# Optimization experiments

Hardware: AMD Instinct MI355X
Metric: run time of the kernel (lower is better)

## Reference

```python
import jax, jax.numpy as jnp
import numpy as np

ALPHA = 0.2          # LeakyReLU slope
NEG_BIG = -9e15      # mask value from the torch code
LN_EPS = 1e-5        # torch LayerNorm default eps
GAT_SCALE = 1.0


def _layer_norm(x, g, b):
    mu = x.mean(-1, keepdims=True)
    var = ((x - mu) ** 2).mean(-1, keepdims=True)
    return (x - mu) * jax.lax.rsqrt(var + LN_EPS) * g + b


def _gat_layer(h, adj, W, a, concat):
    # h: [B,N,Fin], adj: [N,N] weighted, W: [Fin,Fout], a: [2*Fout,1]
    Wh = jnp.einsum('bnf,fo->bno', h, W)                 # [B,N,Fout]
    Fo = W.shape[1]
    a_i, a_j = a[:Fo, 0], a[Fo:, 0]
    # e[b,i,j] = leakyrelu(Wh[b,i].a_i + Wh[b,j].a_j)  (== cat([Wh_i,Wh_j]) @ a)
    e = jax.nn.leaky_relu(
        (Wh @ a_i)[:, :, None] + (Wh @ a_j)[:, None, :], ALPHA)  # [B,N,N]
    att = jnp.where(adj[None, :, :] > 0, e, NEG_BIG)
    att = jax.nn.softmax(att, axis=2)
    att = att * adj[None, :, :]
    att = att / (att.sum(axis=2, keepdims=True) + 1e-8)
    h_prime = jnp.einsum('bij,bjo->bio', att, Wh)        # [B,N,Fout]
    return jax.nn.elu(h_prime) if concat else h_prime


def setup_inputs() -> dict:
    B, N, H, ID = 1024, 128, 64, 8
    GIN = 1 + ID  # node_feat_dim = 0
    key = jax.random.key(0)
    ks = jax.random.split(key, 20)
    # sparse weighted adjacency with self-loops
    w = jax.random.uniform(ks[0], (N, N))
    m = (jax.random.uniform(ks[1], (N, N)) < 0.3).astype(jnp.float32)
    adj = w * m + jnp.eye(N, dtype=jnp.float32)
    sc = lambda k, s: jax.random.normal(k, s, jnp.float32) * 0.1
    return {
        'c_values': jax.random.normal(ks[2], (B, N), jnp.float32),
        'adj': adj,
        'agent_emb': sc(ks[3], (N, ID)),
        'W1': sc(ks[4], (GIN, H)), 'a1': sc(ks[5], (2 * H, 1)),
        'W2': sc(ks[6], (H, H)),   'a2': sc(ks[7], (2 * H, 1)),
        'ln1_g': jnp.ones((H,)), 'ln1_b': jnp.zeros((H,)),
        'ln2_g': jnp.ones((H,)), 'ln2_b': jnp.zeros((H,)),
        'head_gat_w': sc(ks[8], (H, 1)), 'head_gat_b': jnp.zeros((1,)),
        'mlp1_w': sc(ks[9], (N, H)),  'mlp1_b': jnp.zeros((H,)),
        'mlp2_w': sc(ks[10], (H, H)), 'mlp2_b': jnp.zeros((H,)),
        'head_mlp_w': sc(ks[11], (H, 1)), 'head_mlp_b': jnp.zeros((1,)),
        'gate1_w': sc(ks[12], (N, H)), 'gate1_b': jnp.zeros((H,)),
        'gate2_w': sc(ks[13], (H, 1)), 'gate2_b': jnp.full((1,), -5.0),
    }


def reference(c_values, adj, agent_emb, W1, a1, W2, a2,
              ln1_g, ln1_b, ln2_g, ln2_b, head_gat_w, head_gat_b,
              mlp1_w, mlp1_b, mlp2_w, mlp2_b, head_mlp_w, head_mlp_b,
              gate1_w, gate1_b, gate2_w, gate2_b):
    B, N = c_values.shape
    # node features: [c_value, agent_id_embedding]
    id_feat = jnp.broadcast_to(agent_emb[None], (B, N, agent_emb.shape[1]))
    x_g = jnp.concatenate([c_values[..., None], id_feat], axis=-1)  # [B,N,9]
    h1 = _gat_layer(x_g, adj, W1, a1, concat=True)
    h1 = _layer_norm(h1, ln1_g, ln1_b)
    h2 = _gat_layer(h1, adj, W2, a2, concat=False)
    h = jax.nn.relu(h2 + h1)
    h = _layer_norm(h, ln2_g, ln2_b)
    q_gat = h.mean(axis=1) @ head_gat_w + head_gat_b                # [B,1]
    x_m = jax.nn.relu(c_values @ mlp1_w + mlp1_b)
    x_m = jax.nn.relu(x_m @ mlp2_w + mlp2_b)
    q_mlp = x_m @ head_mlp_w + head_mlp_b                           # [B,1]
    gate = jax.nn.sigmoid(
        jax.nn.relu(c_values @ gate1_w + gate1_b) @ gate2_w + gate2_b)
    return q_mlp + gate * GAT_SCALE * q_gat
```

## Files before the change

### kernel.cpp

```cpp
#include <hip/hip_runtime.h>

typedef unsigned short u16;
typedef unsigned int u32;
typedef short v8s __attribute__((ext_vector_type(8)));
typedef float v4f __attribute__((ext_vector_type(4)));

__device__ __forceinline__ float bflo(u32 d){union{u32 i;float f;}u;u.i=d<<16;return u.f;}
__device__ __forceinline__ float bfhi(u32 d){union{u32 i;float f;}u;u.i=d&0xffff0000u;return u.f;}
__device__ __forceinline__ u16 f2bfr(float f){union{float f;u32 i;}u;u.f=f;return (u16)((u.i+0x8000u)>>16);}
__device__ __forceinline__ u32 pk2bf(float a,float b){
    union{float f;u32 i;}ua,ub; ua.f=a; ub.f=b;
    return ((ua.i+0x8000u)>>16)|((ub.i+0x8000u)&0xffff0000u);
}

__device__ __forceinline__ void s_phase(int t, const float* __restrict__ ADJ,
                                        const float* __restrict__ sEi, const float* __restrict__ sEj,
                                        u16* __restrict__ sS, float* __restrict__ sRD)
{
    const int si = t >> 1, jh = (t & 1) * 64;
    const float ei = sEi[si];
    const float4* arow = (const float4*)(ADJ + si * 128 + jh);
    u16* srow = sS + si * 136 + jh;
    float D = 0.f;
    for (int q = 0; q < 8; ++q) {
        float4 a0 = arow[q*2+0];
        float4 a1 = arow[q*2+1];
        const float4* ejp = (const float4*)(sEj + jh + q*8);
        float4 e0 = ejp[0], e1 = ejp[1];
        float av[8] = {a0.x,a0.y,a0.z,a0.w,a1.x,a1.y,a1.z,a1.w};
        float ev[8] = {e0.x,e0.y,e0.z,e0.w,e1.x,e1.y,e1.z,e1.w};
        float w[8];
        #pragma unroll
        for (int k = 0; k < 8; ++k) {
            float e = ei + ev[k];
            e = (e >= 0.f) ? e : 0.2f * e;
            float ww = __expf(e) * av[k];
            ww = (av[k] > 0.f) ? ww : 0.f;
            w[k] = ww;
            D += ww;
        }
        uint4 pk;
        pk.x = pk2bf(w[0], w[1]); pk.y = pk2bf(w[2], w[3]);
        pk.z = pk2bf(w[4], w[5]); pk.w = pk2bf(w[6], w[7]);
        *(uint4*)(srow + q*8) = pk;
    }
    D += __shfl_xor(D, 1);
    if ((t & 1) == 0) sRD[si] = 1.f / D;
}

__device__ __forceinline__ void pv_mfma(const u16* __restrict__ sA, int strA,
                                        const u16* __restrict__ sB, int strB,
                                        int nK, int wv, int l15, int q4, v4f acc[2][4])
{
    #pragma unroll
    for (int ks = 0; ks < 4; ++ks) {
        if (ks >= nK) break;
        const int ko = ks*32 + q4*8;
        v8s A0 = *(const v8s*)(sA + (16*wv     + l15)*strA + ko);
        v8s A1 = *(const v8s*)(sA + (16*(wv+4) + l15)*strA + ko);
        #pragma unroll
        for (int ct = 0; ct < 4; ++ct) {
            v8s B = *(const v8s*)(sB + (16*ct + l15)*strB + ko);
            acc[0][ct] = __builtin_amdgcn_mfma_f32_16x16x32_bf16(A0, B, acc[0][ct], 0,0,0);
            acc[1][ct] = __builtin_amdgcn_mfma_f32_16x16x32_bf16(A1, B, acc[1][ct], 0,0,0);
        }
    }
}

__global__ __launch_bounds__(256, 2) void graphmixer_kernel(
    const float* __restrict__ C,
    const float* __restrict__ ADJ,
    const float* __restrict__ EMB,
    const float* __restrict__ W1,
    const float* __restrict__ A1,
    const float* __restrict__ W2,
    const float* __restrict__ A2,
    const float* __restrict__ LN1G, const float* __restrict__ LN1B,
    const float* __restrict__ LN2G, const float* __restrict__ LN2B,
    const float* __restrict__ HGW,  const float* __restrict__ HGB,
    const float* __restrict__ MLP1W, const float* __restrict__ MLP1B,
    const float* __restrict__ MLP2W, const float* __restrict__ MLP2B,
    const float* __restrict__ HMW,  const float* __restrict__ HMB,
    const float* __restrict__ G1W,  const float* __restrict__ G1B,
    const float* __restrict__ G2W,  const float* __restrict__ G2B,
    float* __restrict__ OUT)
{
    const int b = blockIdx.x, t = threadIdx.x;
    const int lane = t & 63, wv = t >> 6;
    const int l15 = lane & 15, q4 = lane >> 4;

    __shared__ __align__(16) unsigned char smem[74400];
    u16*   sS   = (u16*)(smem);
    u16*   sWhT = (u16*)(smem + 34816);
    u16*   sH1  = (u16*)(smem + 52224);
    float* sEi  = (float*)(smem + 70656);
    float* sEj  = (float*)(smem + 71168);
    float* sRD  = (float*)(smem + 71680);
    float* v2i  = (float*)(smem + 72192);
    float* v2j  = (float*)(smem + 72448);
    float* v1i  = (float*)(smem + 72704);
    float* v1j  = (float*)(smem + 72768);
    float* colp = (float*)(smem + 72832);
    float* sScr = (float*)(smem + 73856);
    float* sEmb = (float*)(smem);
    float* sC   = (float*)(smem + 4096);
    u16*   sW2T = (u16*)(smem);

    ((float4*)sEmb)[t] = ((const float4*)EMB)[t];
    if (t < 32) ((float4*)sC)[t] = ((const float4*)(C + b*128))[t];
    if (t >= 128 && t < 192) {
        int k = t - 128; float a = 0.f;
        for (int q = 0; q < 16; ++q) {
            float4 w = *(const float4*)(W2 + k*64 + q*4);
            float4 x = *(const float4*)(A2 + q*4);
            a += w.x*x.x + w.y*x.y + w.z*x.z + w.w*x.w;
        }
        v2i[k] = a;
    } else if (t >= 192) {
        int k = t - 192; float a = 0.f;
        for (int q = 0; q < 16; ++q) {
            float4 w = *(const float4*)(W2 + k*64 + q*4);
            float4 x = *(const float4*)(A2 + 64 + q*4);
            a += w.x*x.x + w.y*x.y + w.z*x.z + w.w*x.w;
        }
        v2j[k] = a;
    }
    if (t < 9) {
        float a = 0.f;
        for (int q = 0; q < 16; ++q) {
            float4 w = *(const float4*)(W1 + t*64 + q*4);
            float4 x = *(const float4*)(A1 + q*4);
            a += w.x*x.x + w.y*x.y + w.z*x.z + w.w*x.w;
        }
        v1i[t] = a;
    } else if (t >= 16 && t < 25) {
        int f = t - 16; float a = 0.f;
        for (int q = 0; q < 16; ++q) {
            float4 w = *(const float4*)(W1 + f*64 + q*4);
            float4 x = *(const float4*)(A1 + 64 + q*4);
            a += w.x*x.x + w.y*x.y + w.z*x.z + w.w*x.w;
        }
        v1j[f] = a;
    }
    __syncthreads();

    {
        const int o = lane, cc = wv;
        float w1f[9];
        #pragma unroll
        for (int f = 0; f < 9; ++f) w1f[f] = W1[f*64 + o];
        float whv[32];
        for (int i = 0; i < 32; ++i) {
            const int ig = cc*32 + i;
            float a = sC[ig] * w1f[0];
            const float4* ep = (const float4*)(sEmb + ig*8);
            float4 e0 = ep[0], e1 = ep[1];
            a += e0.x*w1f[1] + e0.y*w1f[2] + e0.z*w1f[3] + e0.w*w1f[4];
            a += e1.x*w1f[5] + e1.y*w1f[6] + e1.z*w1f[7] + e1.w*w1f[8];
            whv[i] = a;
        }
        u32 p[16];
        #pragma unroll
        for (int q = 0; q < 16; ++q) p[q] = pk2bf(whv[2*q], whv[2*q+1]);
        uint4* dst = (uint4*)(sWhT + o*136 + cc*32);
        dst[0] = ((uint4*)p)[0]; dst[1] = ((uint4*)p)[1];
        dst[2] = ((uint4*)p)[2]; dst[3] = ((uint4*)p)[3];
    }
    if (t < 128) {
        float c = sC[t];
        const float4* ep = (const float4*)(sEmb + t*8);
        float4 e0 = ep[0], e1 = ep[1];
        float ei = c*v1i[0] + e0.x*v1i[1]+e0.y*v1i[2]+e0.z*v1i[3]+e0.w*v1i[4]
                             + e1.x*v1i[5]+e1.y*v1i[6]+e1.z*v1i[7]+e1.w*v1i[8];
        float ej = c*v1j[0] + e0.x*v1j[1]+e0.y*v1j[2]+e0.z*v1j[3]+e0.w*v1j[4]
                             + e1.x*v1j[5]+e1.y*v1j[6]+e1.z*v1j[7]+e1.w*v1j[8];
        sEi[t] = ei; sEj[t] = ej;
    }
    __syncthreads();

    s_phase(t, ADJ, sEi, sEj, sS, sRD);
    __syncthreads();

    {
        v4f acc[2][4];
        #pragma unroll
        for (int s = 0; s < 2; ++s)
            #pragma unroll
            for (int ct = 0; ct < 4; ++ct) acc[s][ct] = (v4f){0.f,0.f,0.f,0.f};
        pv_mfma(sS, 136, sWhT, 136, 4, wv, l15, q4, acc);

        float g4[4], b4[4];
        #pragma unroll
        for (int ct = 0; ct < 4; ++ct) { g4[ct] = LN1G[16*ct + l15]; b4[ct] = LN1B[16*ct + l15]; }
        #pragma unroll
        for (int s = 0; s < 2; ++s) {
            const int rbase = 16*(wv + 4*s) + 4*q4;
            #pragma unroll
            for (int reg = 0; reg < 4; ++reg) {
                const int row = rbase + reg;
                const float rd = sRD[row];
                float x[4], s1 = 0.f, s2 = 0.f;
                #pragma unroll
                for (int ct = 0; ct < 4; ++ct) {
                    float v = acc[s][ct][reg] * rd;
                    v = (v > 0.f) ? v : (__expf(v) - 1.f);
                    x[ct] = v; s1 += v; s2 += v*v;
                }
                s1 += __shfl_xor(s1, 1); s2 += __shfl_xor(s2, 1);
                s1 += __shfl_xor(s1, 2); s2 += __shfl_xor(s2, 2);
                s1 += __shfl_xor(s1, 4); s2 += __shfl_xor(s2, 4);
                s1 += __shfl_xor(s1, 8); s2 += __shfl_xor(s2, 8);
                const float mean = s1 * (1.f/64.f);
                const float var  = s2 * (1.f/64.f) - mean*mean;
                const float rstd = rsqrtf(var + 1e-5f);
                #pragma unroll
                for (int ct = 0; ct < 4; ++ct) {
                    float h = (x[ct] - mean) * rstd * g4[ct] + b4[ct];
                    sH1[row*72 + 16*ct + l15] = f2bfr(h);
                }
            }
        }
    }
    __syncthreads();

    if (t < 128) {
        float ei = 0.f, ej = 0.f;
        const u16* hrow = sH1 + t*72;
        for (int q = 0; q < 16; ++q) {
            uint2 d = *(const uint2*)(hrow + q*4);
            float h0 = bflo(d.x), h1v = bfhi(d.x), h2 = bflo(d.y), h3 = bfhi(d.y);
            ei += h0*v2i[q*4+0] + h1v*v2i[q*4+1] + h2*v2i[q*4+2] + h3*v2i[q*4+3];
            ej += h0*v2j[q*4+0] + h1v*v2j[q*4+1] + h2*v2j[q*4+2] + h3*v2j[q*4+3];
        }
        sEi[t] = ei; sEj[t] = ej;
    }
    {
        #pragma unroll
        for (int q = 0; q < 4; ++q) {
            float4 v = ((const float4*)W2)[t*4 + q];
            int e = t*16 + q*4;
            int k = e >> 6, n = e & 63;
            sW2T[(n+0)*72 + k] = f2bfr(v.x);
            sW2T[(n+1)*72 + k] = f2bfr(v.y);
            sW2T[(n+2)*72 + k] = f2bfr(v.z);
            sW2T[(n+3)*72 + k] = f2bfr(v.w);
        }
    }
    __syncthreads();

    {
        v4f acc2[2][4];
        #pragma unroll
        for (int s = 0; s < 2; ++s)
            #pragma unroll
            for (int ct = 0; ct < 4; ++ct) acc2[s][ct] = (v4f){0.f,0.f,0.f,0.f};
        pv_mfma(sH1, 72, sW2T, 72, 2, wv, l15, q4, acc2);
        #pragma unroll
        for (int s = 0; s < 2; ++s) {
            const int rb = 16*(wv + 4*s) + 4*q4;
            #pragma unroll
            for (int ct = 0; ct < 4; ++ct) {
                const int col = 16*ct + l15;
                uint2 p;
                p.x = pk2bf(acc2[s][ct][0], acc2[s][ct][1]);
                p.y = pk2bf(acc2[s][ct][2], acc2[s][ct][3]);
                *(uint2*)(sWhT + col*136 + rb) = p;
            }
        }
    }
    __syncthreads();

    s_phase(t, ADJ, sEi, sEj, sS, sRD);
    __syncthreads();

    {
        v4f acc[2][4];
        #pragma unroll
        for (int s = 0; s < 2; ++s)
            #pragma unroll
            for (int ct = 0; ct < 4; ++ct) acc[s][ct] = (v4f){0.f,0.f,0.f,0.f};
        pv_mfma(sS, 136, sWhT, 136, 4, wv, l15, q4, acc);

        float g4[4], b4[4], colsum[4];
        #pragma unroll
        for (int ct = 0; ct < 4; ++ct) {
            g4[ct] = LN2G[16*ct + l15]; b4[ct] = LN2B[16*ct + l15]; colsum[ct] = 0.f;
        }
        #pragma unroll
        for (int s = 0; s < 2; ++s) {
            const int rbase = 16*(wv + 4*s) + 4*q4;
            #pragma unroll
            for (int reg = 0; reg < 4; ++reg) {
                const int row = rbase + reg;
                const float rd = sRD[row];
                float x[4], s1 = 0.f, s2 = 0.f;
                #pragma unroll
                for (int ct = 0; ct < 4; ++ct) {
                    float h1v = bflo((u32)sH1[row*72 + 16*ct + l15]);
                    float v = fmaxf(acc[s][ct][reg] * rd + h1v, 0.f);
                    x[ct] = v; s1 += v; s2 += v*v;
                }
                s1 += __shfl_xor(s1, 1); s2 += __shfl_xor(s2, 1);
                s1 += __shfl_xor(s1, 2); s2 += __shfl_xor(s2, 2);
                s1 += __shfl_xor(s1, 4); s2 += __shfl_xor(s2, 4);
                s1 += __shfl_xor(s1, 8); s2 += __shfl_xor(s2, 8);
                const float mean = s1 * (1.f/64.f);
                const float var  = s2 * (1.f/64.f) - mean*mean;
                const float rstd = rsqrtf(var + 1e-5f);
                #pragma unroll
                for (int ct = 0; ct < 4; ++ct) {
                    float h = (x[ct] - mean) * rstd * g4[ct] + b4[ct];
                    colsum[ct] += h;
                }
            }
        }
        #pragma unroll
        for (int ct = 0; ct < 4; ++ct) {
            colsum[ct] += __shfl_xor(colsum[ct], 16);
            colsum[ct] += __shfl_xor(colsum[ct], 32);
        }
        if (lane < 16) {
            #pragma unroll
            for (int ct = 0; ct < 4; ++ct) colp[wv*64 + ct*16 + lane] = colsum[ct];
        }
    }
    __syncthreads();

    const float* Cb = C + b*128;
    if (wv == 0) {
        float s = colp[lane] + colp[64 + lane] + colp[128 + lane] + colp[192 + lane];
        float p = s * (1.f/128.f) * HGW[lane];
        #pragma unroll
        for (int off = 32; off >= 1; off >>= 1) p += __shfl_down(p, off);
        if (lane == 0) sScr[128] = p + HGB[0];
    } else if (wv == 1) {
        float a = 0.f;
        for (int k = 0; k < 128; k += 4) {
            float4 c4 = *(const float4*)(Cb + k);
            a += c4.x*MLP1W[k*64+lane] + c4.y*MLP1W[(k+1)*64+lane]
               + c4.z*MLP1W[(k+2)*64+lane] + c4.w*MLP1W[(k+3)*64+lane];
        }
        sScr[lane] = fmaxf(a + MLP1B[lane], 0.f);
    } else if (wv == 2) {
        float a = 0.f;
        for (int k = 0; k < 128; k += 4) {
            float4 c4 = *(const float4*)(Cb + k);
            a += c4.x*G1W[k*64+lane] + c4.y*G1W[(k+1)*64+lane]
               + c4.z*G1W[(k+2)*64+lane] + c4.w*G1W[(k+3)*64+lane];
        }
        sScr[64 + lane] = fmaxf(a + G1B[lane], 0.f);
    }
    __syncthreads();

    if (wv == 0) {
        float a = 0.f;
        for (int k = 0; k < 64; ++k) a += sScr[k] * MLP2W[k*64 + lane];
        float x2 = fmaxf(a + MLP2B[lane], 0.f);
        float p1 = x2 * HMW[lane];
        float p2 = sScr[64 + lane] * G2W[lane];
        #pragma unroll
        for (int off = 32; off >= 1; off >>= 1) {
            p1 += __shfl_down(p1, off);
            p2 += __shfl_down(p2, off);
        }
        if (lane == 0) {
            float q_mlp = p1 + HMB[0];
            float gpre  = p2 + G2B[0];
            float gate  = 1.f / (1.f + __expf(-gpre));
            OUT[b] = q_mlp + gate * sScr[128];
        }
    }
}

extern "C" void kernel_launch(void* const* d_in, const int* in_sizes, int n_in,
                              void* d_out, int out_size, void* d_ws, size_t ws_size,
                              hipStream_t stream) {
    (void)n_in; (void)out_size; (void)d_ws; (void)ws_size;
    const float* C     = (const float*)d_in[0];
    const float* ADJ   = (const float*)d_in[1];
    const float* EMB   = (const float*)d_in[2];
    const float* W1    = (const float*)d_in[3];
    const float* A1    = (const float*)d_in[4];
    const float* W2    = (const float*)d_in[5];
    const float* A2    = (const float*)d_in[6];
    const float* LN1G  = (const float*)d_in[7];
    const float* LN1B  = (const float*)d_in[8];
    const float* LN2G  = (const float*)d_in[9];
    const float* LN2B  = (const float*)d_in[10];
    const float* HGW   = (const float*)d_in[11];
    const float* HGB   = (const float*)d_in[12];
    const float* MLP1W = (const float*)d_in[13];
    const float* MLP1B = (const float*)d_in[14];
    const float* MLP2W = (const float*)d_in[15];
    const float* MLP2B = (const float*)d_in[16];
    const float* HMW   = (const float*)d_in[17];
    const float* HMB   = (const float*)d_in[18];
    const float* G1W   = (const float*)d_in[19];
    const float* G1B   = (const float*)d_in[20];
    const float* G2W   = (const float*)d_in[21];
    const float* G2B   = (const float*)d_in[22];

    const int B = in_sizes[0] / 128;

    graphmixer_kernel<<<dim3(B), dim3(256), 0, stream>>>(
        C, ADJ, EMB, W1, A1, W2, A2, LN1G, LN1B, LN2G, LN2B,
        HGW, HGB, MLP1W, MLP1B, MLP2W, MLP2B, HMW, HMB,
        G1W, G1B, G2W, G2B, (float*)d_out);
}
```

Before: 149.4 us.

## Fuse attention scores into MFMA loop and shrink LDS for higher occupancy

New measurement: 129.6 us. -13.2%, faster.

```diff
diff --git a/kernel.cpp b/kernel.cpp
--- a/kernel.cpp
+++ b/kernel.cpp
@@ -12,62 +12,62 @@
     union{float f;u32 i;}ua,ub; ua.f=a; ub.f=b;
     return ((ua.i+0x8000u)>>16)|((ub.i+0x8000u)&0xffff0000u);
 }
-
-__device__ __forceinline__ void s_phase(int t, const float* __restrict__ ADJ,
-                                        const float* __restrict__ sEi, const float* __restrict__ sEj,
-                                        u16* __restrict__ sS, float* __restrict__ sRD)
+__device__ __forceinline__ v8s pack8(const float* w){
+    union { uint4 u; v8s v; } c;
+    c.u.x = pk2bf(w[0],w[1]); c.u.y = pk2bf(w[2],w[3]);
+    c.u.z = pk2bf(w[4],w[5]); c.u.w = pk2bf(w[6],w[7]);
+    return c.v;
+}
+
+__device__ __forceinline__ void flash_att(
+    int wv, int l15, int q4,
+    const float* __restrict__ ADJ,
+    const float* __restrict__ sEi, const float* __restrict__ sEj,
+    const u16* __restrict__ sWhT,
+    v4f acc[2][4], float invD[2])
 {
-    const int si = t >> 1, jh = (t & 1) * 64;
-    const float ei = sEi[si];
-    const float4* arow = (const float4*)(ADJ + si * 128 + jh);
-    u16* srow = sS + si * 136 + jh;
-    float D = 0.f;
-    for (int q = 0; q < 8; ++q) {
-        float4 a0 = arow[q*2+0];
-        float4 a1 = arow[q*2+1];
-        const float4* ejp = (const float4*)(sEj + jh + q*8);
-        float4 e0 = ejp[0], e1 = ejp[1];
-        float av[8] = {a0.x,a0.y,a0.z,a0.w,a1.x,a1.y,a1.z,a1.w};
-        float ev[8] = {e0.x,e0.y,e0.z,e0.w,e1.x,e1.y,e1.z,e1.w};
-        float w[8];
+    const int r0 = 16*wv + l15, r1 = r0 + 64;
+    const float ei0 = sEi[r0], ei1 = sEi[r1];
+    float D0 = 0.f, D1 = 0.f;
+    #pragma unroll
+    for (int s = 0; s < 2; ++s)
+        #pragma unroll
+        for (int ct = 0; ct < 4; ++ct) acc[s][ct] = (v4f){0.f,0.f,0.f,0.f};
+
+    for (int ks = 0; ks < 4; ++ks) {
+        const int ko = ks*32 + q4*8;
+        float ej[8];
+        *(float4*)(ej)     = *(const float4*)(sEj + ko);
+        *(float4*)(ej + 4) = *(const float4*)(sEj + ko + 4);
+        float4 a00 = *(const float4*)(ADJ + r0*128 + ko);
+        float4 a01 = *(const float4*)(ADJ + r0*128 + ko + 4);
+        float4 a10 = *(const float4*)(ADJ + r1*128 + ko);
+        float4 a11 = *(const float4*)(ADJ + r1*128 + ko + 4);
+        float av0[8] = {a00.x,a00.y,a00.z,a00.w,a01.x,a01.y,a01.z,a01.w};
+        float av1[8] = {a10.x,a10.y,a10.z,a10.w,a11.x,a11.y,a11.z,a11.w};
+        float w0[8], w1[8];
         #pragma unroll
         for (int k = 0; k < 8; ++k) {
-            float e = ei + ev[k];
-            e = (e >= 0.f) ? e : 0.2f * e;
-            float ww = __expf(e) * av[k];
-            ww = (av[k] > 0.f) ? ww : 0.f;
-            w[k] = ww;
-            D += ww;
-        }
-        uint4 pk;
-        pk.x = pk2bf(w[0], w[1]); pk.y = pk2bf(w[2], w[3]);
-        pk.z = pk2bf(w[4], w[5]); pk.w = pk2bf(w[6], w[7]);
-        *(uint4*)(srow + q*8) = pk;
-    }
-    D += __shfl_xor(D, 1);
-    if ((t & 1) == 0) sRD[si] = 1.f / D;
-}
-
-__device__ __forceinline__ void pv_mfma(const u16* __restrict__ sA, int strA,
-                                        const u16* __restrict__ sB, int strB,
-                                        int nK, int wv, int l15, int q4, v4f acc[2][4])
-{
-    #pragma unroll
-    for (int ks = 0; ks < 4; ++ks) {
-        if (ks >= nK) break;
-        const int ko = ks*32 + q4*8;
-        v8s A0 = *(const v8s*)(sA + (16*wv     + l15)*strA + ko);
-        v8s A1 = *(const v8s*)(sA + (16*(wv+4) + l15)*strA + ko);
+            float e0 = ei0 + ej[k]; e0 = fmaxf(e0, 0.2f*e0);
+            float e1 = ei1 + ej[k]; e1 = fmaxf(e1, 0.2f*e1);
+            float x0 = __expf(e0) * av0[k];
+            float x1 = __expf(e1) * av1[k];
+            w0[k] = x0; w1[k] = x1; D0 += x0; D1 += x1;
+        }
+        v8s A0 = pack8(w0), A1 = pack8(w1);
         #pragma unroll
         for (int ct = 0; ct < 4; ++ct) {
-            v8s B = *(const v8s*)(sB + (16*ct + l15)*strB + ko);
+            v8s B = *(const v8s*)(sWhT + (16*ct + l15)*136 + ko);
             acc[0][ct] = __builtin_amdgcn_mfma_f32_16x16x32_bf16(A0, B, acc[0][ct], 0,0,0);
             acc[1][ct] = __builtin_amdgcn_mfma_f32_16x16x32_bf16(A1, B, acc[1][ct], 0,0,0);
         }
     }
-}
-
-__global__ __launch_bounds__(256, 2) void graphmixer_kernel(
+    D0 += __shfl_xor(D0, 16); D0 += __shfl_xor(D0, 32);
+    D1 += __shfl_xor(D1, 16); D1 += __shfl_xor(D1, 32);
+    invD[0] = 1.f / D0; invD[1] = 1.f / D1;
+}
+
+__global__ __launch_bounds__(256, 4) void graphmixer_kernel(
     const float* __restrict__ C,
     const float* __restrict__ ADJ,
     const float* __restrict__ EMB,
@@ -89,58 +89,81 @@
     const int lane = t & 63, wv = t >> 6;
     const int l15 = lane & 15, q4 = lane >> 4;
 
-    __shared__ __align__(16) unsigned char smem[74400];
-    u16*   sS   = (u16*)(smem);
-    u16*   sWhT = (u16*)(smem + 34816);
-    u16*   sH1  = (u16*)(smem + 52224);
-    float* sEi  = (float*)(smem + 70656);
-    float* sEj  = (float*)(smem + 71168);
-    float* sRD  = (float*)(smem + 71680);
-    float* v2i  = (float*)(smem + 72192);
-    float* v2j  = (float*)(smem + 72448);
-    float* v1i  = (float*)(smem + 72704);
-    float* v1j  = (float*)(smem + 72768);
-    float* colp = (float*)(smem + 72832);
-    float* sScr = (float*)(smem + 73856);
-    float* sEmb = (float*)(smem);
-    float* sC   = (float*)(smem + 4096);
-    u16*   sW2T = (u16*)(smem);
-
-    ((float4*)sEmb)[t] = ((const float4*)EMB)[t];
-    if (t < 32) ((float4*)sC)[t] = ((const float4*)(C + b*128))[t];
-    if (t >= 128 && t < 192) {
-        int k = t - 128; float a = 0.f;
+    __shared__ __align__(16) unsigned char smem[39072];
+    u16*   sWhT = (u16*)(smem);
+    u16*   sH1  = (u16*)(smem + 17408);
+    float* sEi  = (float*)(smem + 35840);
+    float* sEj  = (float*)(smem + 36352);
+    float* colp = (float*)(smem + 36864);
+    float* sScr = (float*)(smem + 37888);
+    float* v2i  = (float*)(smem + 38432);
+    float* v2j  = (float*)(smem + 38688);
+    float* v1i  = (float*)(smem + 38944);
+    float* v1j  = (float*)(smem + 39008);
+    float* sEmb = (float*)(smem + 17408);
+    float* sC   = (float*)(smem + 21504);
+
+    const float* Cb = C + b*128;
+
+    if (wv == 0) {
+        #pragma unroll
+        for (int q = 0; q < 4; ++q)
+            ((float4*)sEmb)[lane + 64*q] = ((const float4*)EMB)[lane + 64*q];
+        if (lane < 32) ((float4*)sC)[lane] = ((const float4*)Cb)[lane];
+        if (lane >= 32 && lane < 41) {
+            int f = lane - 32; float a = 0.f;
+            for (int q = 0; q < 16; ++q) {
+                float4 w = *(const float4*)(W1 + f*64 + q*4);
+                float4 x = *(const float4*)(A1 + q*4);
+                a += w.x*x.x + w.y*x.y + w.z*x.z + w.w*x.w;
+            }
+            v1i[f] = a;
+        } else if (lane >= 48 && lane < 57) {
+            int f = lane - 48; float a = 0.f;
+            for (int q = 0; q < 16; ++q) {
+                float4 w = *(const float4*)(W1 + f*64 + q*4);
+                float4 x = *(const float4*)(A1 + 64 + q*4);
+                a += w.x*x.x + w.y*x.y + w.z*x.z + w.w*x.w;
+            }
+            v1j[f] = a;
+        }
+    } else if (wv == 3) {
+        float ai = 0.f, aj = 0.f;
         for (int q = 0; q < 16; ++q) {
-            float4 w = *(const float4*)(W2 + k*64 + q*4);
-            float4 x = *(const float4*)(A2 + q*4);
-            a += w.x*x.x + w.y*x.y + w.z*x.z + w.w*x.w;
-        }
-        v2i[k] = a;
-    } else if (t >= 192) {
-        int k = t - 192; float a = 0.f;
-        for (int q = 0; q < 16; ++q) {
-            float4 w = *(const float4*)(W2 + k*64 + q*4);
-            float4 x = *(const float4*)(A2 + 64 + q*4);
-            a += w.x*x.x + w.y*x.y + w.z*x.z + w.w*x.w;
-        }
-        v2j[k] = a;
-    }
-    if (t < 9) {
+            float4 w  = *(const float4*)(W2 + lane*64 + q*4);
+            float4 xi = *(const float4*)(A2 + q*4);
+            float4 xj = *(const float4*)(A2 + 64 + q*4);
+            ai += w.x*xi.x + w.y*xi.y + w.z*xi.z + w.w*xi.w;
+            aj += w.x*xj.x + w.y*xj.y + w.z*xj.z + w.w*xj.w;
+        }
+        v2i[lane] = ai; v2j[lane] = aj;
+    } else if (wv == 1) {
         float a = 0.f;
-        for (int q = 0; q < 16; ++q) {
-            float4 w = *(const float4*)(W1 + t*64 + q*4);
-            float4 x = *(const float4*)(A1 + q*4);
-            a += w.x*x.x + w.y*x.y + w.z*x.z + w.w*x.w;
-        }
-        v1i[t] = a;
-    } else if (t >= 16 && t < 25) {
-        int f = t - 16; float a = 0.f;
-        for (int q = 0; q < 16; ++q) {
-            float4 w = *(const float4*)(W1 + f*64 + q*4);
-            float4 x = *(const float4*)(A1 + 64 + q*4);
-            a += w.x*x.x + w.y*x.y + w.z*x.z + w.w*x.w;
-        }
-        v1j[f] = a;
+        for (int k = 0; k < 128; k += 4) {
+            float4 c4 = *(const float4*)(Cb + k);
+            a += c4.x*MLP1W[k*64+lane] + c4.y*MLP1W[(k+1)*64+lane]
+               + c4.z*MLP1W[(k+2)*64+lane] + c4.w*MLP1W[(k+3)*64+lane];
+        }
+        sScr[lane] = fmaxf(a + MLP1B[lane], 0.f);
+        float a2 = 0.f;
+        for (int k = 0; k < 64; ++k) a2 += sScr[k] * MLP2W[k*64 + lane];
+        float x2 = fmaxf(a2 + MLP2B[lane], 0.f);
+        float p1 = x2 * HMW[lane];
+        #pragma unroll
+        for (int off = 32; off >= 1; off >>= 1) p1 += __shfl_down(p1, off);
+        if (lane == 0) sScr[128] = p1 + HMB[0];
+    } else {
+        float a = 0.f;
+        for (int k = 0; k < 128; k += 4) {
+            float4 c4 = *(const float4*)(Cb + k);
+            a += c4.x*G1W[k*64+lane] + c4.y*G1W[(k+1)*64+lane]
+               + c4.z*G1W[(k+2)*64+lane] + c4.w*G1W[(k+3)*64+lane];
+        }
+        sScr[64 + lane] = fmaxf(a + G1B[lane], 0.f);
+        float p2 = sScr[64 + lane] * G2W[lane];
+        #pragma unroll
+        for (int off = 32; off >= 1; off >>= 1) p2 += __shfl_down(p2, off);
+        if (lane == 0) sScr[129] = 1.f / (1.f + __expf(-(p2 + G2B[0])));
     }
     __syncthreads();
 
@@ -153,8 +176,8 @@
         for (int i = 0; i < 32; ++i) {
             const int ig = cc*32 + i;
             float a = sC[ig] * w1f[0];
-            const float4* ep = (const float4*)(sEmb + ig*8);
-            float4 e0 = ep[0], e1 = ep[1];
+            float4 e0 = *(const float4*)(sEmb + ig*8);
+            float4 e1 = *(const float4*)(sEmb + ig*8 + 4);
             a += e0.x*w1f[1] + e0.y*w1f[2] + e0.z*w1f[3] + e0.w*w1f[4];
             a += e1.x*w1f[5] + e1.y*w1f[6] + e1.z*w1f[7] + e1.w*w1f[8];
             whv[i] = a;
@@ -168,26 +191,19 @@
     }
     if (t < 128) {
         float c = sC[t];
-        const float4* ep = (const float4*)(sEmb + t*8);
-        float4 e0 = ep[0], e1 = ep[1];
+        float4 e0 = *(const float4*)(sEmb + t*8);
+        float4 e1 = *(const float4*)(sEmb + t*8 + 4);
         float ei = c*v1i[0] + e0.x*v1i[1]+e0.y*v1i[2]+e0.z*v1i[3]+e0.w*v1i[4]
-                             + e1.x*v1i[5]+e1.y*v1i[6]+e1.z*v1i[7]+e1.w*v1i[8];
+                            + e1.x*v1i[5]+e1.y*v1i[6]+e1.z*v1i[7]+e1.w*v1i[8];
         float ej = c*v1j[0] + e0.x*v1j[1]+e0.y*v1j[2]+e0.z*v1j[3]+e0.w*v1j[4]
-                             + e1.x*v1j[5]+e1.y*v1j[6]+e1.z*v1j[7]+e1.w*v1j[8];
+                            + e1.x*v1j[5]+e1.y*v1j[6]+e1.z*v1j[7]+e1.w*v1j[8];
         sEi[t] = ei; sEj[t] = ej;
     }
     __syncthreads();
 
-    s_phase(t, ADJ, sEi, sEj, sS, sRD);
-    __syncthreads();
-
     {
-        v4f acc[2][4];
-        #pragma unroll
-        for (int s = 0; s < 2; ++s)
-            #pragma unroll
-            for (int ct = 0; ct < 4; ++ct) acc[s][ct] = (v4f){0.f,0.f,0.f,0.f};
-        pv_mfma(sS, 136, sWhT, 136, 4, wv, l15, q4, acc);
+        v4f acc[2][4]; float invD[2];
+        flash_att(wv, l15, q4, ADJ, sEi, sEj, sWhT, acc, invD);
 
         float g4[4], b4[4];
         #pragma unroll
@@ -198,7 +214,7 @@
             #pragma unroll
             for (int reg = 0; reg < 4; ++reg) {
                 const int row = rbase + reg;
-                const float rd = sRD[row];
+                const float rd = __shfl(invD[s], 4*q4 + reg);
                 float x[4], s1 = 0.f, s2 = 0.f;
                 #pragma unroll
                 for (int ct = 0; ct < 4; ++ct) {
@@ -235,29 +251,34 @@
         sEi[t] = ei; sEj[t] = ej;
     }
     {
-        #pragma unroll
-        for (int q = 0; q < 4; ++q) {
-            float4 v = ((const float4*)W2)[t*4 + q];
-            int e = t*16 + q*4;
-            int k = e >> 6, n = e & 63;
-            sW2T[(n+0)*72 + k] = f2bfr(v.x);
-            sW2T[(n+1)*72 + k] = f2bfr(v.y);
-            sW2T[(n+2)*72 + k] = f2bfr(v.z);
-            sW2T[(n+3)*72 + k] = f2bfr(v.w);
-        }
-    }
-    __syncthreads();
-
-    {
         v4f acc2[2][4];
         #pragma unroll
         for (int s = 0; s < 2; ++s)
             #pragma unroll
             for (int ct = 0; ct < 4; ++ct) acc2[s][ct] = (v4f){0.f,0.f,0.f,0.f};
-        pv_mfma(sH1, 72, sW2T, 72, 2, wv, l15, q4, acc2);
+        #pragma unroll
+        for (int ks = 0; ks < 2; ++ks) {
+            const int kb = ks*32 + q4*8;
+            v8s Bf[4];
+            #pragma unroll
+            for (int ct = 0; ct < 4; ++ct) {
+                const float* wp = W2 + kb*64 + 16*ct + l15;
+                float w8[8];
+                #pragma unroll
+                for (int j = 0; j < 8; ++j) w8[j] = wp[j*64];
+                Bf[ct] = pack8(w8);
+            }
+            #pragma unroll
+            for (int s = 0; s < 2; ++s) {
+                v8s A = *(const v8s*)(sH1 + (16*(wv+4*s) + l15)*72 + kb);
+                #pragma unroll
+                for (int ct = 0; ct < 4; ++ct)
+                    acc2[s][ct] = __builtin_amdgcn_mfma_f32_16x16x32_bf16(A, Bf[ct], acc2[s][ct], 0,0,0);
+            }
+        }
         #pragma unroll
         for (int s = 0; s < 2; ++s) {
-            const int rb = 16*(wv + 4*s) + 4*q4;
+            const int rb = 16*(wv+4*s) + 4*q4;
             #pragma unroll
             for (int ct = 0; ct < 4; ++ct) {
                 const int col = 16*ct + l15;
@@ -270,16 +291,9 @@
     }
     __syncthreads();
 
-    s_phase(t, ADJ, sEi, sEj, sS, sRD);
-    __syncthreads();
-
     {
-        v4f acc[2][4];
-        #pragma unroll
-        for (int s = 0; s < 2; ++s)
-            #pragma unroll
-            for (int ct = 0; ct < 4; ++ct) acc[s][ct] = (v4f){0.f,0.f,0.f,0.f};
-        pv_mfma(sS, 136, sWhT, 136, 4, wv, l15, q4, acc);
+        v4f acc[2][4]; float invD[2];
+        flash_att(wv, l15, q4, ADJ, sEi, sEj, sWhT, acc, invD);
 
         float g4[4], b4[4], colsum[4];
         #pragma unroll
@@ -292,7 +306,7 @@
             #pragma unroll
             for (int reg = 0; reg < 4; ++reg) {
                 const int row = rbase + reg;
-                const float rd = sRD[row];
+                const float rd = __shfl(invD[s], 4*q4 + reg);
                 float x[4], s1 = 0.f, s2 = 0.f;
                 #pragma unroll
                 for (int ct = 0; ct < 4; ++ct) {
@@ -308,10 +322,8 @@
                 const float var  = s2 * (1.f/64.f) - mean*mean;
                 const float rstd = rsqrtf(var + 1e-5f);
                 #pragma unroll
-                for (int ct = 0; ct < 4; ++ct) {
-                    float h = (x[ct] - mean) * rstd * g4[ct] + b4[ct];
-                    colsum[ct] += h;
-                }
+                for (int ct = 0; ct < 4; ++ct)
+                    colsum[ct] += (x[ct] - mean) * rstd * g4[ct] + b4[ct];
             }
         }
         #pragma unroll
@@ -326,49 +338,12 @@
     }
     __syncthreads();
 
-    const float* Cb = C + b*128;
     if (wv == 0) {
         float s = colp[lane] + colp[64 + lane] + colp[128 + lane] + colp[192 + lane];
         float p = s * (1.f/128.f) * HGW[lane];
         #pragma unroll
         for (int off = 32; off >= 1; off >>= 1) p += __shfl_down(p, off);
-        if (lane == 0) sScr[128] = p + HGB[0];
-    } else if (wv == 1) {
-        float a = 0.f;
-        for (int k = 0; k < 128; k += 4) {
-            float4 c4 = *(const float4*)(Cb + k);
-            a += c4.x*MLP1W[k*64+lane] + c4.y*MLP1W[(k+1)*64+lane]
-               + c4.z*MLP1W[(k+2)*64+lane] + c4.w*MLP1W[(k+3)*64+lane];
-        }
-        sScr[lane] = fmaxf(a + MLP1B[lane], 0.f);
-    } else if (wv == 2) {
-        float a = 0.f;
-        for (int k = 0; k < 128; k += 4) {
-            float4 c4 = *(const float4*)(Cb + k);
-            a += c4.x*G1W[k*64+lane] + c4.y*G1W[(k+1)*64+lane]
-               + c4.z*G1W[(k+2)*64+lane] + c4.w*G1W[(k+3)*64+lane];
-        }
-        sScr[64 + lane] = fmaxf(a + G1B[lane], 0.f);
-    }
-    __syncthreads();
-
-    if (wv == 0) {
-        float a = 0.f;
-        for (int k = 0; k < 64; ++k) a += sScr[k] * MLP2W[k*64 + lane];
-        float x2 = fmaxf(a + MLP2B[lane], 0.f);
-        float p1 = x2 * HMW[lane];
-        float p2 = sScr[64 + lane] * G2W[lane];
-        #pragma unroll
-        for (int off = 32; off >= 1; off >>= 1) {
-            p1 += __shfl_down(p1, off);
-            p2 += __shfl_down(p2, off);
-        }
-        if (lane == 0) {
-            float q_mlp = p1 + HMB[0];
-            float gpre  = p2 + G2B[0];
-            float gate  = 1.f / (1.f + __expf(-gpre));
-            OUT[b] = q_mlp + gate * sScr[128];
-        }
+        if (lane == 0) OUT[b] = sScr[128] + sScr[129] * (p + HGB[0]);
     }
 }
 
```
